# Optimization experiments

Measured on AMD Instinct MI355X. Metric: run time of the kernel, lower is better.

The kernel has to match this reference:

```python
import jax, jax.numpy as jnp
import numpy as np

NB, C, S = 3, 20, 7          # num_boxes, num_classes, gridsize
D = 5 * NB + C               # per-cell channel count = 35
B = 8192


def setup_inputs() -> dict:
    key = jax.random.key(0)
    k1, k2, k3 = jax.random.split(key, 3)
    output = jax.random.uniform(k1, (B, S, S, D), dtype=jnp.float32) * 0.9 + 0.05
    target = jax.random.uniform(k2, (B, S, S, D), dtype=jnp.float32) * 0.9 + 0.05
    # conf channel must be exactly 0 or 1 (obj_mask: conf==1, noobj_mask: conf==0)
    conf = (jax.random.uniform(k3, (B, S, S)) < 0.15).astype(jnp.float32)
    conf_idx = 5 * jnp.arange(NB) + 4          # indices 4, 9, 14
    target = target.at[..., conf_idx].set(conf[..., None])
    return {"output": output, "target": target}


def _to_xyxy(b):
    # b[..., :4] = (cx, cy, w, h); cx,cy are grid-relative (divided by gridsize)
    xy = b[..., :2] / S
    half = 0.5 * b[..., 2:4]
    return jnp.concatenate([xy - half, xy + half], axis=-1)


def reference(output, target):
    nB = output.shape[0]
    out = output.reshape(-1, D)                  # [N, D], N = B*S*S
    tgt = target.reshape(-1, D)
    pbox = out[:, :5 * NB].reshape(-1, NB, 5)    # [N, NB, 5]
    tbox = tgt[:, :5 * NB].reshape(-1, NB, 5)
    pcls = out[:, 5 * NB:]                       # [N, C]
    tcls = tgt[:, 5 * NB:]
    conf_t = tgt[:, 4]
    obj = (conf_t == 1.0).astype(out.dtype)      # [N]
    noobj = (conf_t == 0.0).astype(out.dtype)

    # IoU of each predicted box vs the (single) target box of its cell
    p_xyxy = _to_xyxy(pbox)                      # [N, NB, 4]
    t_xyxy = _to_xyxy(tbox[:, 0, :])[:, None, :] # [N, 1, 4]
    lt = jnp.maximum(p_xyxy[..., :2], t_xyxy[..., :2])
    rb = jnp.minimum(p_xyxy[..., 2:], t_xyxy[..., 2:])
    wh = jnp.clip(rb - lt, 0.0)
    inter = wh[..., 0] * wh[..., 1]              # [N, NB]
    a1 = (p_xyxy[..., 2] - p_xyxy[..., 0]) * (p_xyxy[..., 3] - p_xyxy[..., 1])
    a2 = (t_xyxy[..., 2] - t_xyxy[..., 0]) * (t_xyxy[..., 3] - t_xyxy[..., 1])
    iou = inter / (a1 + a2 - inter)
    best = jnp.argmax(iou, axis=1)               # responsible box index per cell
    max_iou = jnp.max(iou, axis=1)               # [N]
    resp = jax.nn.one_hot(best, NB, dtype=out.dtype) * obj[:, None]  # [N, NB]

    xy_loss = jnp.sum(resp * jnp.sum((pbox[..., :2] - tbox[..., :2]) ** 2, -1))
    wh_loss = jnp.sum(resp * jnp.sum((jnp.sqrt(pbox[..., 2:4]) - jnp.sqrt(tbox[..., 2:4])) ** 2, -1))
    contain_loss = jnp.sum(resp * (pbox[..., 4] - max_iou[:, None]) ** 2)
    class_loss = jnp.sum(obj[:, None] * (pcls - tcls) ** 2)
    noobj_conf_loss = jnp.sum(noobj[:, None] * (pbox[..., 4] - tbox[..., 4]) ** 2)

    coord_scale, noobject_scale = 5.0, 0.5
    return (coord_scale * (xy_loss + wh_loss) + contain_loss
            + noobject_scale * noobj_conf_loss + class_loss) / nB
```

## Files before the change

kernel.cpp:

```cpp
#include <hip/hip_runtime.h>


#define NBOX 3
#define NCLS 20
#define SDIM 7
#define DCH  35
#define NTHREADS 256

typedef float float4u __attribute__((ext_vector_type(4), aligned(4)));

__global__ __launch_bounds__(NTHREADS) void detloss_kernel(
    const float* __restrict__ out_g, const float* __restrict__ tgt_g,
    float* __restrict__ partials, float inv_nB)
{
    __shared__ float s_part[NTHREADS / 64];

    const int tid  = threadIdx.x;
    const long long cell = (long long)blockIdx.x * NTHREADS + tid;
    const float* ob = out_g + cell * DCH;
    const float* gb = tgt_g + cell * DCH;

    float o[36], g[36];
    #pragma unroll
    for (int k = 0; k < 8; ++k) {
        *(float4u*)&o[4 * k] = *(const float4u*)(ob + 4 * k);
        *(float4u*)&g[4 * k] = *(const float4u*)(gb + 4 * k);
    }
    {
        float4u to = *(const float4u*)(ob + 31);
        float4u tg = *(const float4u*)(gb + 31);
        o[31] = to.x; o[32] = to.y; o[33] = to.z; o[34] = to.w;
        g[31] = tg.x; g[32] = tg.y; g[33] = tg.z; g[34] = tg.w;
    }

    const float tx  = g[0] / 7.0f, ty = g[1] / 7.0f;
    const float thw = 0.5f * g[2], thh = 0.5f * g[3];
    const float tx1 = tx - thw, ty1 = ty - thh;
    const float tx2 = tx + thw, ty2 = ty + thh;
    const float a2  = (tx2 - tx1) * (ty2 - ty1);

    const float conf_t = g[4];
    const float obj    = (conf_t == 1.0f) ? 1.0f : 0.0f;
    const float noobj  = (conf_t == 0.0f) ? 1.0f : 0.0f;

    float biou = -__builtin_inff();
    float conf_sq = 0.0f;
    float bo0 = 0.f, bo1 = 0.f, bo2 = 0.f, bo3 = 0.f, bo4 = 0.f;
    float bg0 = 0.f, bg1 = 0.f, bg2 = 0.f, bg3 = 0.f;

    #pragma unroll
    for (int i = 0; i < NBOX; ++i) {
        const float px  = o[5*i]   / 7.0f;
        const float py  = o[5*i+1] / 7.0f;
        const float phw = 0.5f * o[5*i+2];
        const float phh = 0.5f * o[5*i+3];
        const float px1 = px - phw, py1 = py - phh;
        const float px2 = px + phw, py2 = py + phh;

        const float ltx = fmaxf(px1, tx1), lty = fmaxf(py1, ty1);
        const float rbx = fminf(px2, tx2), rby = fminf(py2, ty2);
        const float w = fmaxf(rbx - ltx, 0.0f);
        const float h = fmaxf(rby - lty, 0.0f);
        const float inter = w * h;
        const float a1 = (px2 - px1) * (py2 - py1);
        const float iou = inter / (a1 + a2 - inter);

        const bool better = iou > biou;
        biou = better ? iou      : biou;
        bo0  = better ? o[5*i]   : bo0;
        bo1  = better ? o[5*i+1] : bo1;
        bo2  = better ? o[5*i+2] : bo2;
        bo3  = better ? o[5*i+3] : bo3;
        bo4  = better ? o[5*i+4] : bo4;
        bg0  = better ? g[5*i]   : bg0;
        bg1  = better ? g[5*i+1] : bg1;
        bg2  = better ? g[5*i+2] : bg2;
        bg3  = better ? g[5*i+3] : bg3;

        const float dc = o[5*i+4] - g[5*i+4];
        conf_sq += dc * dc;
    }

    float loss = 0.5f * noobj * conf_sq;

    const float dx = bo0 - bg0;
    const float dy = bo1 - bg1;
    const float xyl = dx*dx + dy*dy;
    const float dw = sqrtf(bo2) - sqrtf(bg2);
    const float dh = sqrtf(bo3) - sqrtf(bg3);
    const float whl = dw*dw + dh*dh;
    const float dcf = bo4 - biou;
    const float contain = dcf * dcf;

    float cls = 0.0f;
    #pragma unroll
    for (int c = 0; c < NCLS; ++c) {
        const float d = o[5*NBOX + c] - g[5*NBOX + c];
        cls += d * d;
    }

    loss += obj * (5.0f * (xyl + whl) + contain + cls);
    loss *= inv_nB;

    #pragma unroll
    for (int off = 32; off > 0; off >>= 1)
        loss += __shfl_down(loss, off);
    if ((tid & 63) == 0) s_part[tid >> 6] = loss;
    __syncthreads();
    if (tid == 0) {
        float tot = s_part[0];
        #pragma unroll
        for (int w = 1; w < NTHREADS / 64; ++w) tot += s_part[w];
        partials[blockIdx.x] = tot;
    }
}

__global__ __launch_bounds__(1024) void reduce_kernel(
    const float* __restrict__ partials, float* __restrict__ out, int n)
{
    __shared__ float s[1024 / 64];
    float v = 0.0f;
    for (int i = threadIdx.x; i < n; i += 1024) v += partials[i];
    #pragma unroll
    for (int off = 32; off > 0; off >>= 1)
        v += __shfl_down(v, off);
    if ((threadIdx.x & 63) == 0) s[threadIdx.x >> 6] = v;
    __syncthreads();
    if (threadIdx.x == 0) {
        float t = 0.0f;
        #pragma unroll
        for (int w = 0; w < 1024 / 64; ++w) t += s[w];
        out[0] = t;
    }
}

extern "C" void kernel_launch(void* const* d_in, const int* in_sizes, int n_in,
                              void* d_out, int out_size, void* d_ws, size_t ws_size,
                              hipStream_t stream) {
    const float* out_p = (const float*)d_in[0];
    const float* tgt_p = (const float*)d_in[1];
    float* res  = (float*)d_out;
    float* part = (float*)d_ws;

    const int n_cells = in_sizes[0] / DCH;
    const int nB = n_cells / (SDIM * SDIM);
    const float inv_nB = 1.0f / (float)nB;

    const int blocks = n_cells / NTHREADS;
    hipLaunchKernelGGL(detloss_kernel, dim3(blocks), dim3(NTHREADS), 0, stream,
                       out_p, tgt_p, part, inv_nB);
    hipLaunchKernelGGL(reduce_kernel, dim3(1), dim3(1024), 0, stream,
                       part, res, blocks);
}
```

Before: 148.3 us.

## Stage cell tiles through LDS with coalesced loads in persistent single-wave blocks

Each 64-thread block now loads a tile of 64 cells for both tensors with contiguous float4 reads into LDS. Lanes then read their 35-float cell from LDS; the odd stride avoids bank conflicts. The previous per-thread strided loads touched poorly coalesced 140-byte records. A persistent grid of 2048 single-wave blocks loops over tiles and prefetches the next tile into registers while computing the current one. The block reduction shrinks to a single wave shuffle. Risks are lower occupancy and heavy register use from the 18 float4 prefetch registers.

```diff
diff --git a/kernel.cpp b/kernel.cpp
--- a/kernel.cpp
+++ b/kernel.cpp
@@ -5,114 +5,130 @@
 #define NCLS 20
 #define SDIM 7
 #define DCH  35
-#define NTHREADS 256
+#define TILE_F4 560
+#define FLAT_F4 (2 * TILE_F4)
+#define LDS_F4  1152
 
-typedef float float4u __attribute__((ext_vector_type(4), aligned(4)));
+__global__ __launch_bounds__(64) void detloss_kernel(
+    const float* __restrict__ out_g, const float* __restrict__ tgt_g,
+    float* __restrict__ partials, int n_tiles, float inv_nB)
+{
+    __shared__ float4 s_buf[LDS_F4];
 
-__global__ __launch_bounds__(NTHREADS) void detloss_kernel(
-    const float* __restrict__ out_g, const float* __restrict__ tgt_g,
-    float* __restrict__ partials, float inv_nB)
-{
-    __shared__ float s_part[NTHREADS / 64];
+    const int lane = threadIdx.x;
+    const int wid  = blockIdx.x;
+    const int nwv  = gridDim.x;
 
-    const int tid  = threadIdx.x;
-    const long long cell = (long long)blockIdx.x * NTHREADS + tid;
-    const float* ob = out_g + cell * DCH;
-    const float* gb = tgt_g + cell * DCH;
+    float4 r[18];
+    float lane_sum = 0.0f;
 
-    float o[36], g[36];
-    #pragma unroll
-    for (int k = 0; k < 8; ++k) {
-        *(float4u*)&o[4 * k] = *(const float4u*)(ob + 4 * k);
-        *(float4u*)&g[4 * k] = *(const float4u*)(gb + 4 * k);
-    }
-    {
-        float4u to = *(const float4u*)(ob + 31);
-        float4u tg = *(const float4u*)(gb + 31);
-        o[31] = to.x; o[32] = to.y; o[33] = to.z; o[34] = to.w;
-        g[31] = tg.x; g[32] = tg.y; g[33] = tg.z; g[34] = tg.w;
+    auto load_tile = [&](int tile) {
+        const float4* go = (const float4*)out_g + (long long)tile * TILE_F4;
+        const float4* gt = (const float4*)tgt_g + (long long)tile * TILE_F4;
+        #pragma unroll
+        for (int j = 0; j < 18; ++j) {
+            int k = j * 64 + lane;
+            k = (k > FLAT_F4 - 1) ? (FLAT_F4 - 1) : k;
+            r[j] = (k < TILE_F4) ? go[k] : gt[k - TILE_F4];
+        }
+    };
+
+    auto store_tile = [&]() {
+        #pragma unroll
+        for (int j = 0; j < 18; ++j)
+            s_buf[j * 64 + lane] = r[j];
+    };
+
+    auto compute = [&]() {
+        const float* sf = (const float*)s_buf;
+        const float* o  = sf + lane * DCH;
+        const float* g  = sf + 4 * TILE_F4 + lane * DCH;
+
+        const float tx  = g[0] / 7.0f, ty = g[1] / 7.0f;
+        const float thw = 0.5f * g[2], thh = 0.5f * g[3];
+        const float tx1 = tx - thw, ty1 = ty - thh;
+        const float tx2 = tx + thw, ty2 = ty + thh;
+        const float a2  = (tx2 - tx1) * (ty2 - ty1);
+
+        const float conf_t = g[4];
+        const float obj    = (conf_t == 1.0f) ? 1.0f : 0.0f;
+        const float noobj  = (conf_t == 0.0f) ? 1.0f : 0.0f;
+
+        float biou = -__builtin_inff();
+        float conf_sq = 0.0f;
+        float bo0 = 0.f, bo1 = 0.f, bo2 = 0.f, bo3 = 0.f, bo4 = 0.f;
+        float bg0 = 0.f, bg1 = 0.f, bg2 = 0.f, bg3 = 0.f;
+
+        #pragma unroll
+        for (int i = 0; i < NBOX; ++i) {
+            const float px  = o[5*i]   / 7.0f;
+            const float py  = o[5*i+1] / 7.0f;
+            const float phw = 0.5f * o[5*i+2];
+            const float phh = 0.5f * o[5*i+3];
+            const float px1 = px - phw, py1 = py - phh;
+            const float px2 = px + phw, py2 = py + phh;
+
+            const float ltx = fmaxf(px1, tx1), lty = fmaxf(py1, ty1);
+            const float rbx = fminf(px2, tx2), rby = fminf(py2, ty2);
+            const float w = fmaxf(rbx - ltx, 0.0f);
+            const float h = fmaxf(rby - lty, 0.0f);
+            const float inter = w * h;
+            const float a1 = (px2 - px1) * (py2 - py1);
+            const float iou = inter / (a1 + a2 - inter);
+
+            const bool better = iou > biou;
+            biou = better ? iou      : biou;
+            bo0  = better ? o[5*i]   : bo0;
+            bo1  = better ? o[5*i+1] : bo1;
+            bo2  = better ? o[5*i+2] : bo2;
+            bo3  = better ? o[5*i+3] : bo3;
+            bo4  = better ? o[5*i+4] : bo4;
+            bg0  = better ? g[5*i]   : bg0;
+            bg1  = better ? g[5*i+1] : bg1;
+            bg2  = better ? g[5*i+2] : bg2;
+            bg3  = better ? g[5*i+3] : bg3;
+
+            const float dc = o[5*i+4] - g[5*i+4];
+            conf_sq += dc * dc;
+        }
+
+        float loss = 0.5f * noobj * conf_sq;
+
+        const float dx = bo0 - bg0;
+        const float dy = bo1 - bg1;
+        const float xyl = dx*dx + dy*dy;
+        const float dw = sqrtf(bo2) - sqrtf(bg2);
+        const float dh = sqrtf(bo3) - sqrtf(bg3);
+        const float whl = dw*dw + dh*dh;
+        const float dcf = bo4 - biou;
+        const float contain = dcf * dcf;
+
+        float cls = 0.0f;
+        #pragma unroll
+        for (int c = 0; c < NCLS; ++c) {
+            const float d = o[5*NBOX + c] - g[5*NBOX + c];
+            cls += d * d;
+        }
+
+        lane_sum += loss + obj * (5.0f * (xyl + whl) + contain + cls);
+    };
+
+    if (wid < n_tiles) {
+        load_tile(wid);
+        store_tile();
+        for (int nxt = wid + nwv; nxt < n_tiles; nxt += nwv) {
+            load_tile(nxt);
+            compute();
+            store_tile();
+        }
+        compute();
     }
 
-    const float tx  = g[0] / 7.0f, ty = g[1] / 7.0f;
-    const float thw = 0.5f * g[2], thh = 0.5f * g[3];
-    const float tx1 = tx - thw, ty1 = ty - thh;
-    const float tx2 = tx + thw, ty2 = ty + thh;
-    const float a2  = (tx2 - tx1) * (ty2 - ty1);
-
-    const float conf_t = g[4];
-    const float obj    = (conf_t == 1.0f) ? 1.0f : 0.0f;
-    const float noobj  = (conf_t == 0.0f) ? 1.0f : 0.0f;
-
-    float biou = -__builtin_inff();
-    float conf_sq = 0.0f;
-    float bo0 = 0.f, bo1 = 0.f, bo2 = 0.f, bo3 = 0.f, bo4 = 0.f;
-    float bg0 = 0.f, bg1 = 0.f, bg2 = 0.f, bg3 = 0.f;
-
-    #pragma unroll
-    for (int i = 0; i < NBOX; ++i) {
-        const float px  = o[5*i]   / 7.0f;
-        const float py  = o[5*i+1] / 7.0f;
-        const float phw = 0.5f * o[5*i+2];
-        const float phh = 0.5f * o[5*i+3];
-        const float px1 = px - phw, py1 = py - phh;
-        const float px2 = px + phw, py2 = py + phh;
-
-        const float ltx = fmaxf(px1, tx1), lty = fmaxf(py1, ty1);
-        const float rbx = fminf(px2, tx2), rby = fminf(py2, ty2);
-        const float w = fmaxf(rbx - ltx, 0.0f);
-        const float h = fmaxf(rby - lty, 0.0f);
-        const float inter = w * h;
-        const float a1 = (px2 - px1) * (py2 - py1);
-        const float iou = inter / (a1 + a2 - inter);
-
-        const bool better = iou > biou;
-        biou = better ? iou      : biou;
-        bo0  = better ? o[5*i]   : bo0;
-        bo1  = better ? o[5*i+1] : bo1;
-        bo2  = better ? o[5*i+2] : bo2;
-        bo3  = better ? o[5*i+3] : bo3;
-        bo4  = better ? o[5*i+4] : bo4;
-        bg0  = better ? g[5*i]   : bg0;
-        bg1  = better ? g[5*i+1] : bg1;
-        bg2  = better ? g[5*i+2] : bg2;
-        bg3  = better ? g[5*i+3] : bg3;
-
-        const float dc = o[5*i+4] - g[5*i+4];
-        conf_sq += dc * dc;
-    }
-
-    float loss = 0.5f * noobj * conf_sq;
-
-    const float dx = bo0 - bg0;
-    const float dy = bo1 - bg1;
-    const float xyl = dx*dx + dy*dy;
-    const float dw = sqrtf(bo2) - sqrtf(bg2);
-    const float dh = sqrtf(bo3) - sqrtf(bg3);
-    const float whl = dw*dw + dh*dh;
-    const float dcf = bo4 - biou;
-    const float contain = dcf * dcf;
-
-    float cls = 0.0f;
-    #pragma unroll
-    for (int c = 0; c < NCLS; ++c) {
-        const float d = o[5*NBOX + c] - g[5*NBOX + c];
-        cls += d * d;
-    }
-
-    loss += obj * (5.0f * (xyl + whl) + contain + cls);
-    loss *= inv_nB;
-
+    float v = lane_sum * inv_nB;
     #pragma unroll
     for (int off = 32; off > 0; off >>= 1)
-        loss += __shfl_down(loss, off);
-    if ((tid & 63) == 0) s_part[tid >> 6] = loss;
-    __syncthreads();
-    if (tid == 0) {
-        float tot = s_part[0];
-        #pragma unroll
-        for (int w = 1; w < NTHREADS / 64; ++w) tot += s_part[w];
-        partials[blockIdx.x] = tot;
-    }
+        v += __shfl_down(v, off);
+    if (lane == 0) partials[wid] = v;
 }
 
 __global__ __launch_bounds__(1024) void reduce_kernel(
@@ -145,10 +161,11 @@
     const int n_cells = in_sizes[0] / DCH;
     const int nB = n_cells / (SDIM * SDIM);
     const float inv_nB = 1.0f / (float)nB;
+    const int n_tiles = n_cells / 64;
 
-    const int blocks = n_cells / NTHREADS;
-    hipLaunchKernelGGL(detloss_kernel, dim3(blocks), dim3(NTHREADS), 0, stream,
-                       out_p, tgt_p, part, inv_nB);
+    const int nblocks = 2048;
+    hipLaunchKernelGGL(detloss_kernel, dim3(nblocks), dim3(64), 0, stream,
+                       out_p, tgt_p, part, n_tiles, inv_nB);
     hipLaunchKernelGGL(reduce_kernel, dim3(1), dim3(1024), 0, stream,
-                       part, res, blocks);
+                       part, res, nblocks);
 }
```

After: 164.9 us. 11.2% more time.

## Coalesce cell loads per wave via float4 tiles and shared-memory scatter

Applied to the files above, without the earlier changes.

Each 64-lane wave now loads a contiguous tile of 64 cells as coalesced float4 vectors instead of each thread reading its own strided 35-float record. The elementwise squared differences (class and no-object confidence terms) are accumulated directly from the loaded vectors. Only the 15 box channels per cell are scattered into LDS for the per-cell IoU pass. Per-wave partials replace the block-level LDS reduction. This targets uncoalesced global access, at the cost of extra index arithmetic, LDS traffic and twice as many partials for the final reduce.

```diff
diff --git a/kernel.cpp b/kernel.cpp
--- a/kernel.cpp
+++ b/kernel.cpp
@@ -1,59 +1,112 @@
 #include <hip/hip_runtime.h>
 
 
-#define NBOX 3
-#define NCLS 20
-#define SDIM 7
 #define DCH  35
-#define NTHREADS 256
+#define TILE_F4 560
 
-typedef float float4u __attribute__((ext_vector_type(4), aligned(4)));
-
-__global__ __launch_bounds__(NTHREADS) void detloss_kernel(
+__global__ __launch_bounds__(128, 4) void detloss_kernel(
     const float* __restrict__ out_g, const float* __restrict__ tgt_g,
     float* __restrict__ partials, float inv_nB)
 {
-    __shared__ float s_part[NTHREADS / 64];
+    __shared__ float s_o[2][960];
+    __shared__ float s_g[2][960];
 
-    const int tid  = threadIdx.x;
-    const long long cell = (long long)blockIdx.x * NTHREADS + tid;
-    const float* ob = out_g + cell * DCH;
-    const float* gb = tgt_g + cell * DCH;
+    const int lane = threadIdx.x & 63;
+    const int wv   = threadIdx.x >> 6;
+    const int tile = blockIdx.x * 2 + wv;
 
-    float o[36], g[36];
-    #pragma unroll
-    for (int k = 0; k < 8; ++k) {
-        *(float4u*)&o[4 * k] = *(const float4u*)(ob + 4 * k);
-        *(float4u*)&g[4 * k] = *(const float4u*)(gb + 4 * k);
-    }
-    {
-        float4u to = *(const float4u*)(ob + 31);
-        float4u tg = *(const float4u*)(gb + 31);
-        o[31] = to.x; o[32] = to.y; o[33] = to.z; o[34] = to.w;
-        g[31] = tg.x; g[32] = tg.y; g[33] = tg.z; g[34] = tg.w;
-    }
+    float* __restrict__ so = s_o[wv];
+    float* __restrict__ sg = s_g[wv];
 
-    const float tx  = g[0] / 7.0f, ty = g[1] / 7.0f;
-    const float thw = 0.5f * g[2], thh = 0.5f * g[3];
+    const float4* go = (const float4*)out_g + (long long)tile * TILE_F4;
+    const float4* gt = (const float4*)tgt_g + (long long)tile * TILE_F4;
+
+    float4 o0,o1,o2,o3,o4,o5,o6,o7,o8;
+    float4 g0,g1,g2,g3,g4,g5,g6,g7,g8;
+    float ew_acc = 0.0f;
+
+#define ISSUE(J, OJ, GJ) do {                                   \
+        const int k_ = (J)*64 + lane;                           \
+        if ((J) < 8 || lane < 48) { OJ = go[k_]; GJ = gt[k_]; } \
+    } while (0)
+
+    ISSUE(0,o0,g0); ISSUE(1,o1,g1); ISSUE(2,o2,g2); ISSUE(3,o3,g3);
+    ISSUE(4,o4,g4); ISSUE(5,o5,g5); ISSUE(6,o6,g6); ISSUE(7,o7,g7);
+    ISSUE(8,o8,g8);
+
+#define SCAT1(OV, GV) do {                                      \
+        if (c_ < 15u) { unsigned a_ = cell_*15u + c_;           \
+            so[a_] = (OV); sg[a_] = (GV); }                     \
+        c_++; if (c_ == 35u) { c_ = 0u; cell_++; }              \
+    } while (0)
+
+#define SCATTER(J, OJ, GJ) do {                                 \
+        if ((J) < 8 || lane < 48) {                             \
+            unsigned e_ = 4u*(unsigned)((J)*64 + lane);         \
+            unsigned cell_ = e_ / 35u;                          \
+            unsigned c_ = e_ - cell_*35u;                       \
+            SCAT1(OJ.x, GJ.x); SCAT1(OJ.y, GJ.y);               \
+            SCAT1(OJ.z, GJ.z); SCAT1(OJ.w, GJ.w);               \
+            OJ.x -= GJ.x; OJ.x *= OJ.x;                         \
+            OJ.y -= GJ.y; OJ.y *= OJ.y;                         \
+            OJ.z -= GJ.z; OJ.z *= OJ.z;                         \
+            OJ.w -= GJ.w; OJ.w *= OJ.w;                         \
+        }                                                       \
+    } while (0)
+
+    SCATTER(0,o0,g0); SCATTER(1,o1,g1); SCATTER(2,o2,g2); SCATTER(3,o3,g3);
+    SCATTER(4,o4,g4); SCATTER(5,o5,g5); SCATTER(6,o6,g6); SCATTER(7,o7,g7);
+    SCATTER(8,o8,g8);
+
+#define WSEL(C, OBJ, NO) ((C) >= 15u ? (OBJ) : (((C)==4u || (C)==9u || (C)==14u) ? (NO) : 0.0f))
+#define ACC1(D2) do {                                           \
+        ew_acc += WSEL(c_, objc_, noc_) * (D2);                 \
+        c_++; if (c_ == 35u) { c_ = 0u; objc_ = obj1_; noc_ = no1_; } \
+    } while (0)
+
+#define ACCUM(J, OJ) do {                                       \
+        if ((J) < 8 || lane < 48) {                             \
+            unsigned e_ = 4u*(unsigned)((J)*64 + lane);         \
+            unsigned cell_ = e_ / 35u;                          \
+            unsigned c_ = e_ - cell_*35u;                       \
+            const float f0_ = sg[cell_*15u + 4u];               \
+            const float f1_ = (c_ >= 32u) ? sg[(cell_+1u)*15u + 4u] : f0_; \
+            const float obj0_ = (f0_ == 1.0f) ? 1.0f : 0.0f;    \
+            const float no0_  = (f0_ == 0.0f) ? 0.5f : 0.0f;    \
+            const float obj1_ = (f1_ == 1.0f) ? 1.0f : 0.0f;    \
+            const float no1_  = (f1_ == 0.0f) ? 0.5f : 0.0f;    \
+            float objc_ = obj0_, noc_ = no0_;                   \
+            ACC1(OJ.x); ACC1(OJ.y); ACC1(OJ.z); ACC1(OJ.w);     \
+        }                                                       \
+    } while (0)
+
+    ACCUM(0,o0); ACCUM(1,o1); ACCUM(2,o2); ACCUM(3,o3);
+    ACCUM(4,o4); ACCUM(5,o5); ACCUM(6,o6); ACCUM(7,o7);
+    ACCUM(8,o8);
+
+    const float* oc = so + lane * 15;
+    const float* gc = sg + lane * 15;
+
+    const float tx  = gc[0] / 7.0f, ty = gc[1] / 7.0f;
+    const float thw = 0.5f * gc[2], thh = 0.5f * gc[3];
     const float tx1 = tx - thw, ty1 = ty - thh;
     const float tx2 = tx + thw, ty2 = ty + thh;
     const float a2  = (tx2 - tx1) * (ty2 - ty1);
 
-    const float conf_t = g[4];
+    const float conf_t = gc[4];
     const float obj    = (conf_t == 1.0f) ? 1.0f : 0.0f;
-    const float noobj  = (conf_t == 0.0f) ? 1.0f : 0.0f;
 
     float biou = -__builtin_inff();
-    float conf_sq = 0.0f;
     float bo0 = 0.f, bo1 = 0.f, bo2 = 0.f, bo3 = 0.f, bo4 = 0.f;
     float bg0 = 0.f, bg1 = 0.f, bg2 = 0.f, bg3 = 0.f;
 
     #pragma unroll
-    for (int i = 0; i < NBOX; ++i) {
-        const float px  = o[5*i]   / 7.0f;
-        const float py  = o[5*i+1] / 7.0f;
-        const float phw = 0.5f * o[5*i+2];
-        const float phh = 0.5f * o[5*i+3];
+    for (int i = 0; i < 3; ++i) {
+        const float ox = oc[5*i], oy = oc[5*i+1], ow = oc[5*i+2], oh = oc[5*i+3];
+        const float px  = ox / 7.0f;
+        const float py  = oy / 7.0f;
+        const float phw = 0.5f * ow;
+        const float phh = 0.5f * oh;
         const float px1 = px - phw, py1 = py - phh;
         const float px2 = px + phw, py2 = py + phh;
 
@@ -66,22 +119,17 @@
         const float iou = inter / (a1 + a2 - inter);
 
         const bool better = iou > biou;
-        biou = better ? iou      : biou;
-        bo0  = better ? o[5*i]   : bo0;
-        bo1  = better ? o[5*i+1] : bo1;
-        bo2  = better ? o[5*i+2] : bo2;
-        bo3  = better ? o[5*i+3] : bo3;
-        bo4  = better ? o[5*i+4] : bo4;
-        bg0  = better ? g[5*i]   : bg0;
-        bg1  = better ? g[5*i+1] : bg1;
-        bg2  = better ? g[5*i+2] : bg2;
-        bg3  = better ? g[5*i+3] : bg3;
-
-        const float dc = o[5*i+4] - g[5*i+4];
-        conf_sq += dc * dc;
+        biou = better ? iou        : biou;
+        bo0  = better ? ox         : bo0;
+        bo1  = better ? oy         : bo1;
+        bo2  = better ? ow         : bo2;
+        bo3  = better ? oh         : bo3;
+        bo4  = better ? oc[5*i+4]  : bo4;
+        bg0  = better ? gc[5*i]    : bg0;
+        bg1  = better ? gc[5*i+1]  : bg1;
+        bg2  = better ? gc[5*i+2]  : bg2;
+        bg3  = better ? gc[5*i+3]  : bg3;
     }
-
-    float loss = 0.5f * noobj * conf_sq;
 
     const float dx = bo0 - bg0;
     const float dy = bo1 - bg1;
@@ -92,27 +140,12 @@
     const float dcf = bo4 - biou;
     const float contain = dcf * dcf;
 
-    float cls = 0.0f;
-    #pragma unroll
-    for (int c = 0; c < NCLS; ++c) {
-        const float d = o[5*NBOX + c] - g[5*NBOX + c];
-        cls += d * d;
-    }
-
-    loss += obj * (5.0f * (xyl + whl) + contain + cls);
-    loss *= inv_nB;
+    float v = (ew_acc + obj * (5.0f * (xyl + whl) + contain)) * inv_nB;
 
     #pragma unroll
     for (int off = 32; off > 0; off >>= 1)
-        loss += __shfl_down(loss, off);
-    if ((tid & 63) == 0) s_part[tid >> 6] = loss;
-    __syncthreads();
-    if (tid == 0) {
-        float tot = s_part[0];
-        #pragma unroll
-        for (int w = 1; w < NTHREADS / 64; ++w) tot += s_part[w];
-        partials[blockIdx.x] = tot;
-    }
+        v += __shfl_down(v, off);
+    if (lane == 0) partials[tile] = v;
 }
 
 __global__ __launch_bounds__(1024) void reduce_kernel(
@@ -143,12 +176,13 @@
     float* part = (float*)d_ws;
 
     const int n_cells = in_sizes[0] / DCH;
-    const int nB = n_cells / (SDIM * SDIM);
+    const int nB = n_cells / 49;
     const float inv_nB = 1.0f / (float)nB;
+    const int n_tiles = n_cells / 64;
+    const int blocks  = n_tiles / 2;
 
-    const int blocks = n_cells / NTHREADS;
-    hipLaunchKernelGGL(detloss_kernel, dim3(blocks), dim3(NTHREADS), 0, stream,
+    hipLaunchKernelGGL(detloss_kernel, dim3(blocks), dim3(128), 0, stream,
                        out_p, tgt_p, part, inv_nB);
     hipLaunchKernelGGL(reduce_kernel, dim3(1), dim3(1024), 0, stream,
-                       part, res, blocks);
+                       part, res, n_tiles);
 }
```

Measured after the change: 133.8 us. -9.8%, faster.
